# Kernel optimization log

Hardware: AMD Instinct MI355X
Metric: run time of the kernel (lower is better)

Reference implementation:

```python
import jax, jax.numpy as jnp
import numpy as np

MODEL_DIM = 512
NUM_HEADS = 8
HEAD_DIM = MODEL_DIM // NUM_HEADS  # 64
NUM_NODE = 1024
CLUSTER = 128
S = 60
EMBED = 0.5


def setup_inputs() -> dict:
    key = jax.random.key(0)
    ks = jax.random.split(key, 16)
    d = MODEL_DIM
    sc = 1.0 / np.sqrt(d)
    inp = {
        "x": jax.random.normal(ks[0], (4, 12, NUM_NODE, d), dtype=jnp.float32),
        "Wq": jax.random.normal(ks[1], (d, d), dtype=jnp.float32) * sc,
        "bq": jnp.zeros((d,), jnp.float32),
        "Wk": jax.random.normal(ks[2], (d, d), dtype=jnp.float32) * sc,
        "bk": jnp.zeros((d,), jnp.float32),
        "Wv": jax.random.normal(ks[3], (d, d), dtype=jnp.float32) * sc,
        "bv": jnp.zeros((d,), jnp.float32),
        "We": jax.random.normal(ks[4], (d, d), dtype=jnp.float32) * sc,
        "be": jnp.zeros((d,), jnp.float32),
        "Wo": jax.random.normal(ks[5], (d, d), dtype=jnp.float32) * sc,
        "bo": jnp.zeros((d,), jnp.float32),
        # adp_pos is initialized to zeros in torch; use small randn for a non-degenerate test
        "adp_pos": jax.random.normal(ks[6], (NUM_NODE, CLUSTER), dtype=jnp.float32) * 0.02,
        "U1": jax.random.normal(ks[7], (HEAD_DIM, S), dtype=jnp.float32) * np.sqrt(2.0 / (HEAD_DIM + S)),
        "U2": jax.random.normal(ks[8], (S, HEAD_DIM), dtype=jnp.float32) * np.sqrt(2.0 / (S + HEAD_DIM)),
    }
    return inp


def _split_heads(t):
    # torch.cat(torch.split(t, head_dim, -1), 0): heads stacked head-major on batch dim
    return jnp.concatenate(jnp.split(t, NUM_HEADS, axis=-1), axis=0)


def _merge_heads(t):
    return jnp.concatenate(jnp.split(t, NUM_HEADS, axis=0), axis=-1)


def _pool_nodes(t):
    # AdaptiveAvgPool2d((CLUSTER, None)) on (B,T,N,D) with N % CLUSTER == 0 -> block mean
    B, T, N, D = t.shape
    return t.reshape(B, T, CLUSTER, N // CLUSTER, D).mean(axis=3)


def reference(x, Wq, bq, Wk, bk, Wv, bv, We, be, Wo, bo, adp_pos, U1, U2):
    q = x @ Wq.T + bq                      # (B,T,N,D)
    k = _pool_nodes(x @ Wk.T + bk)          # (B,T,C,D)
    v = _pool_nodes(x @ Wv.T + bv)          # (B,T,C,D)
    ev = x @ We.T + be                      # (B,T,N,D)

    qh = _split_heads(q)                    # (B*H,T,N,d)
    kh = _split_heads(k)                    # (B*H,T,C,d)
    vh = _split_heads(v)                    # (B*H,T,C,d)
    evh = _split_heads(ev)                  # (B*H,T,N,d)

    # external attention branch: softmax over node dim (-2)
    exa = jax.nn.softmax(evh @ U1, axis=-2)  # (B*H,T,N,S)
    exa_val = (exa @ U2) * EMBED + evh       # (B*H,T,N,d)

    score = jnp.einsum("btnd,btcd->btnc", qh, kh) / np.sqrt(HEAD_DIM)
    score = score + adp_pos[None, None]      # (B*H,T,N,C)
    attn = jax.nn.softmax(score, axis=-1)

    out = attn @ vh + exa_val                # (B*H,T,N,d)
    out = _merge_heads(out)                  # (B,T,N,D)
    return out @ Wo.T + bo
```

## Files before the change

kernel.cpp:

```cpp
#include <hip/hip_runtime.h>


#define LOG2E 1.44269504088896f

typedef __attribute__((ext_vector_type(4))) float f32x4;
typedef __attribute__((ext_vector_type(8))) short bf16x8;

__device__ __forceinline__ unsigned short f2bf(float f) {
    union { float f; unsigned u; } v; v.f = f;
    unsigned r = (v.u + 0x7fffu + ((v.u >> 16) & 1u)) >> 16;
    return (unsigned short)r;
}
__device__ __forceinline__ float bf2f(unsigned short h) {
    union { unsigned u; float f; } v; v.u = ((unsigned)h) << 16;
    return v.f;
}
__device__ __forceinline__ unsigned cvt_pk_bf16(float lo, float hi) {
    unsigned r;
    asm("v_cvt_pk_bf16_f32 %0, %1, %2" : "=v"(r) : "v"(lo), "v"(hi));
    return r;
}
__device__ __forceinline__ void gll16(const void* g, void* l) {
    __builtin_amdgcn_global_load_lds((const __attribute__((address_space(1))) void*)g,
                                     (__attribute__((address_space(3))) void*)l,
                                     16, 0, 0);
}

__global__ void cvt_w(const float* __restrict__ Wq, const float* __restrict__ Wk,
                      const float* __restrict__ Wv, const float* __restrict__ We,
                      const float* __restrict__ Wo, const float* __restrict__ U1,
                      const float* __restrict__ U2,
                      const float* __restrict__ bq, const float* __restrict__ bk,
                      const float* __restrict__ bv, const float* __restrict__ be,
                      unsigned short* __restrict__ Wqe, unsigned short* __restrict__ Wkv,
                      unsigned short* __restrict__ Wob, unsigned short* __restrict__ U1T,
                      unsigned short* __restrict__ U2bT,
                      float* __restrict__ bqe, float* __restrict__ bkv)
{
    int i = blockIdx.x * 256 + threadIdx.x;
    if (i < 524288) {
        int r = i >> 9;
        float v = (r < 512) ? Wq[i] * 0.125f : We[i - 262144];
        Wqe[i] = f2bf(v);
    } else if (i < 1048576) {
        int j = i - 524288; int r = j >> 9;
        float v = (r < 512) ? Wk[j] : Wv[j - 262144];
        Wkv[j] = f2bf(v);
    } else if (i < 1310720) {
        int j = i - 1048576;
        Wob[j] = f2bf(Wo[j]);
    } else if (i < 1314816) {
        int j = i - 1310720; int s = j >> 6, k = j & 63;
        U1T[j] = (s < 60) ? f2bf(U1[k * 60 + s]) : (unsigned short)0;
    } else if (i < 1318912) {
        int j = i - 1314816; int d = j >> 6, s = j & 63;
        U2bT[j] = (s < 60) ? f2bf(U2[s * 64 + d] * 0.5f) : (unsigned short)0;
    } else if (i < 1319936) {
        int j = i - 1318912;
        bqe[j] = (j < 512) ? bq[j] * 0.125f : be[j - 512];
    } else if (i < 1320960) {
        int j = i - 1319936;
        bkv[j] = (j < 512) ? bk[j] : bv[j - 512];
    }
}

__global__ void cvt_pool(const float* __restrict__ x, unsigned short* __restrict__ xb,
                         unsigned short* __restrict__ xpb)
{
    int i = blockIdx.x * 256 + threadIdx.x;
    int d4 = i & 127;
    int btc = i >> 7;
    int bt = btc >> 7, c = btc & 127;
    long base = ((long)(bt * 1024 + c * 8)) * 128 + d4;
    const float4* src = (const float4*)x + base;
    ushort4* dst = (ushort4*)xb + base;
    float sx = 0.f, sy = 0.f, sz = 0.f, sw = 0.f;
#pragma unroll
    for (int j = 0; j < 8; j++) {
        float4 v = src[(long)j * 128];
        sx += v.x; sy += v.y; sz += v.z; sw += v.w;
        ushort4 o;
        o.x = f2bf(v.x); o.y = f2bf(v.y); o.z = f2bf(v.z); o.w = f2bf(v.w);
        dst[(long)j * 128] = o;
    }
    ushort4 p;
    p.x = f2bf(sx * 0.125f); p.y = f2bf(sy * 0.125f);
    p.z = f2bf(sz * 0.125f); p.w = f2bf(sw * 0.125f);
    ((ushort4*)xpb)[(long)btc * 128 + d4] = p;
}

__global__ __launch_bounds__(256, 4) void g1_qev(
    const unsigned short* __restrict__ A, const unsigned short* __restrict__ W,
    const float* __restrict__ bias, unsigned short* __restrict__ qh,
    unsigned short* __restrict__ evh)
{
    const int K = 512;
    __shared__ __attribute__((aligned(16))) unsigned short As[128 * 32];
    __shared__ __attribute__((aligned(16))) unsigned short Bs[128 * 32];
    const int tid = threadIdx.x;
    const int wave = tid >> 6, lane = tid & 63;
    const int quad = lane >> 4, l16 = lane & 15;
    const int m0 = blockIdx.x * 128, n0 = blockIdx.y * 128;
    const int wm = (wave & 1) * 64, wn = (wave >> 1) * 64;

    f32x4 acc[4][4];
#pragma unroll
    for (int i = 0; i < 4; i++)
#pragma unroll
        for (int j = 0; j < 4; j++) acc[i][j] = (f32x4){0.f, 0.f, 0.f, 0.f};

    const int c0 = tid, c1 = tid + 256;
    const int r0 = c0 >> 2, kc0 = (c0 & 3) * 8;
    const int r1 = c1 >> 2, kc1 = (c1 & 3) * 8;
    const unsigned short* pa0 = A + (long)(m0 + r0) * K + kc0;
    const unsigned short* pa1 = A + (long)(m0 + r1) * K + kc1;
    const unsigned short* pb0 = W + (long)(n0 + r0) * K + kc0;
    const unsigned short* pb1 = W + (long)(n0 + r1) * K + kc1;
    unsigned short* lA0 = &As[wave * 512];
    unsigned short* lA1 = &As[2048 + wave * 512];
    unsigned short* lB0 = &Bs[wave * 512];
    unsigned short* lB1 = &Bs[2048 + wave * 512];

    for (int k0 = 0; k0 < K; k0 += 32) {
        gll16(pa0 + k0, lA0);
        gll16(pa1 + k0, lA1);
        gll16(pb0 + k0, lB0);
        gll16(pb1 + k0, lB1);
        __syncthreads();
        bf16x8 af[4], bfr[4];
#pragma unroll
        for (int t = 0; t < 4; t++)
            af[t] = *(const bf16x8*)&As[(wm + t * 16 + l16) * 32 + quad * 8];
#pragma unroll
        for (int t = 0; t < 4; t++)
            bfr[t] = *(const bf16x8*)&Bs[(wn + t * 16 + l16) * 32 + quad * 8];
#pragma unroll
        for (int tm = 0; tm < 4; tm++)
#pragma unroll
            for (int tn = 0; tn < 4; tn++)
                acc[tm][tn] = __builtin_amdgcn_mfma_f32_16x16x32_bf16(
                    af[tm], bfr[tn], acc[tm][tn], 0, 0, 0);
        __syncthreads();
    }

#pragma unroll
    for (int tm = 0; tm < 4; tm++)
#pragma unroll
        for (int tn = 0; tn < 4; tn++) {
            int cc = n0 + wn + tn * 16 + l16;
            float bv = bias[cc];
            int hq = (cc >> 6) & 7, dd = cc & 63;
            int rr0 = m0 + wm + tm * 16 + quad * 4;
            int bt = rr0 >> 10, n = rr0 & 1023;
            unsigned short* dst = ((cc < 512) ? qh : evh)
                + ((long)(bt * 8 + hq) * 1024 + n) * 64 + dd;
#pragma unroll
            for (int r = 0; r < 4; r++)
                dst[(long)r * 64] = f2bf(acc[tm][tn][r] + bv);
        }
}

template <int OUTF32>
__global__ __launch_bounds__(256, 4) void gemm_bt(
    const unsigned short* __restrict__ A, const unsigned short* __restrict__ W,
    const float* __restrict__ bias, void* __restrict__ Cout,
    int M, int N, int K)
{
    __shared__ __attribute__((aligned(16))) unsigned short As[128 * 32];
    __shared__ __attribute__((aligned(16))) unsigned short Bs[128 * 32];
    const int tid = threadIdx.x;
    const int wave = tid >> 6, lane = tid & 63;
    const int quad = lane >> 4, l16 = lane & 15;
    const int m0 = blockIdx.x * 128, n0 = blockIdx.y * 128;
    const int wm = (wave & 1) * 64, wn = (wave >> 1) * 64;

    f32x4 acc[4][4];
#pragma unroll
    for (int i = 0; i < 4; i++)
#pragma unroll
        for (int j = 0; j < 4; j++) acc[i][j] = (f32x4){0.f, 0.f, 0.f, 0.f};

    const int c0 = tid, c1 = tid + 256;
    const int r0 = c0 >> 2, kc0 = (c0 & 3) * 8;
    const int r1 = c1 >> 2, kc1 = (c1 & 3) * 8;
    const unsigned short* pa0 = A + (long)(m0 + r0) * K + kc0;
    const unsigned short* pa1 = A + (long)(m0 + r1) * K + kc1;
    const unsigned short* pb0 = W + (long)(n0 + r0) * K + kc0;
    const unsigned short* pb1 = W + (long)(n0 + r1) * K + kc1;
    unsigned short* lA0 = &As[wave * 512];
    unsigned short* lA1 = &As[2048 + wave * 512];
    unsigned short* lB0 = &Bs[wave * 512];
    unsigned short* lB1 = &Bs[2048 + wave * 512];

    for (int k0 = 0; k0 < K; k0 += 32) {
        gll16(pa0 + k0, lA0);
        gll16(pa1 + k0, lA1);
        gll16(pb0 + k0, lB0);
        gll16(pb1 + k0, lB1);
        __syncthreads();
        bf16x8 af[4], bfr[4];
#pragma unroll
        for (int t = 0; t < 4; t++)
            af[t] = *(const bf16x8*)&As[(wm + t * 16 + l16) * 32 + quad * 8];
#pragma unroll
        for (int t = 0; t < 4; t++)
            bfr[t] = *(const bf16x8*)&Bs[(wn + t * 16 + l16) * 32 + quad * 8];
#pragma unroll
        for (int tm = 0; tm < 4; tm++)
#pragma unroll
            for (int tn = 0; tn < 4; tn++)
                acc[tm][tn] = __builtin_amdgcn_mfma_f32_16x16x32_bf16(
                    af[tm], bfr[tn], acc[tm][tn], 0, 0, 0);
        __syncthreads();
    }

#pragma unroll
    for (int tm = 0; tm < 4; tm++)
#pragma unroll
        for (int tn = 0; tn < 4; tn++) {
            int cc = n0 + wn + tn * 16 + l16;
            float bv = bias[cc];
#pragma unroll
            for (int r = 0; r < 4; r++) {
                int rr = m0 + wm + tm * 16 + quad * 4 + r;
                float v = acc[tm][tn][r] + bv;
                if (OUTF32) ((float*)Cout)[(long)rr * N + cc] = v;
                else        ((unsigned short*)Cout)[(long)rr * N + cc] = f2bf(v);
            }
        }
}

__global__ __launch_bounds__(256, 4) void g2_kv(
    const unsigned short* __restrict__ A, const unsigned short* __restrict__ W,
    const float* __restrict__ bias, unsigned short* __restrict__ kvK,
    unsigned short* __restrict__ vT)
{
    const int K = 512;
    __shared__ __attribute__((aligned(16))) unsigned short As[128 * 32];
    __shared__ __attribute__((aligned(16))) unsigned short Bs[128 * 32];
    const int tid = threadIdx.x;
    const int wave = tid >> 6, lane = tid & 63;
    const int quad = lane >> 4, l16 = lane & 15;
    const int m0 = blockIdx.x * 128, n0 = blockIdx.y * 128;
    const int wm = (wave & 1) * 64, wn = (wave >> 1) * 64;

    f32x4 acc[4][4];
#pragma unroll
    for (int i = 0; i < 4; i++)
#pragma unroll
        for (int j = 0; j < 4; j++) acc[i][j] = (f32x4){0.f, 0.f, 0.f, 0.f};

    const int c0 = tid, c1 = tid + 256;
    const int r0 = c0 >> 2, kc0 = (c0 & 3) * 8;
    const int r1 = c1 >> 2, kc1 = (c1 & 3) * 8;
    const unsigned short* pa0 = A + (long)(m0 + r0) * K + kc0;
    const unsigned short* pa1 = A + (long)(m0 + r1) * K + kc1;
    const unsigned short* pb0 = W + (long)(n0 + r0) * K + kc0;
    const unsigned short* pb1 = W + (long)(n0 + r1) * K + kc1;
    unsigned short* lA0 = &As[wave * 512];
    unsigned short* lA1 = &As[2048 + wave * 512];
    unsigned short* lB0 = &Bs[wave * 512];
    unsigned short* lB1 = &Bs[2048 + wave * 512];

    for (int k0 = 0; k0 < K; k0 += 32) {
        gll16(pa0 + k0, lA0);
        gll16(pa1 + k0, lA1);
        gll16(pb0 + k0, lB0);
        gll16(pb1 + k0, lB1);
        __syncthreads();
        bf16x8 af[4], bfr[4];
#pragma unroll
        for (int t = 0; t < 4; t++)
            af[t] = *(const bf16x8*)&As[(wm + t * 16 + l16) * 32 + quad * 8];
#pragma unroll
        for (int t = 0; t < 4; t++)
            bfr[t] = *(const bf16x8*)&Bs[(wn + t * 16 + l16) * 32 + quad * 8];
#pragma unroll
        for (int tm = 0; tm < 4; tm++)
#pragma unroll
            for (int tn = 0; tn < 4; tn++)
                acc[tm][tn] = __builtin_amdgcn_mfma_f32_16x16x32_bf16(
                    af[tm], bfr[tn], acc[tm][tn], 0, 0, 0);
        __syncthreads();
    }

#pragma unroll
    for (int tm = 0; tm < 4; tm++)
#pragma unroll
        for (int tn = 0; tn < 4; tn++) {
            int cc = n0 + wn + tn * 16 + l16;
            float bv = bias[cc];
            int rrb = m0 + wm + tm * 16 + quad * 4;
            if (cc < 512) {
#pragma unroll
                for (int r = 0; r < 4; r++)
                    kvK[(long)(rrb + r) * 512 + cc] = f2bf(acc[tm][tn][r] + bv);
            } else {
                int hh = (cc - 512) >> 6, dd = (cc - 512) & 63;
                int btv = rrb >> 7, cv = rrb & 127;
                ushort4 o;
                o.x = f2bf(acc[tm][tn][0] + bv);
                o.y = f2bf(acc[tm][tn][1] + bv);
                o.z = f2bf(acc[tm][tn][2] + bv);
                o.w = f2bf(acc[tm][tn][3] + bv);
                *(ushort4*)(vT + ((long)(btv * 8 + hh) * 64 + dd) * 128 + cv) = o;
            }
        }
}

__global__ __launch_bounds__(256, 2) void ez_kernel(
    const unsigned short* __restrict__ evh, const unsigned short* __restrict__ U1T,
    unsigned short* __restrict__ Z)
{
    __shared__ __attribute__((aligned(16))) unsigned short evs[128 * 72];
    __shared__ __attribute__((aligned(16))) unsigned short u1s[64 * 72];
    int tid = threadIdx.x, bx = blockIdx.x;
    int bt = bx >> 6, h = (bx >> 3) & 7, nb = bx & 7;
    int wave = tid >> 6, lane = tid & 63, quad = lane >> 4, l16 = lane & 15;
    long gb = ((long)(bt * 8 + h) * 1024 + nb * 128) * 64;

#pragma unroll
    for (int i = 0; i < 4; i++) {
        int c = tid + i * 256; int row = c >> 3, kc = (c & 7) * 8;
        *(int4*)&evs[row * 72 + kc] = *(const int4*)(evh + gb + row * 64 + kc);
    }
#pragma unroll
    for (int i = 0; i < 2; i++) {
        int c = tid + i * 256; int row = c >> 3, kc = (c & 7) * 8;
        *(int4*)&u1s[row * 72 + kc] = *(const int4*)(U1T + row * 64 + kc);
    }
    __syncthreads();

    f32x4 acc[2][4];
#pragma unroll
    for (int i = 0; i < 2; i++)
#pragma unroll
        for (int t = 0; t < 4; t++) acc[i][t] = (f32x4){0.f, 0.f, 0.f, 0.f};

#pragma unroll
    for (int kt = 0; kt < 2; kt++) {
        bf16x8 a[2], b[4];
#pragma unroll
        for (int i = 0; i < 2; i++)
            a[i] = *(const bf16x8*)&evs[((wave * 2 + i) * 16 + l16) * 72 + kt * 32 + quad * 8];
#pragma unroll
        for (int t = 0; t < 4; t++)
            b[t] = *(const bf16x8*)&u1s[(t * 16 + l16) * 72 + kt * 32 + quad * 8];
#pragma unroll
        for (int i = 0; i < 2; i++)
#pragma unroll
            for (int t = 0; t < 4; t++)
                acc[i][t] = __builtin_amdgcn_mfma_f32_16x16x32_bf16(a[i], b[t], acc[i][t], 0, 0, 0);
    }

    long zb = (long)(bt * 8 + h) * 1024 + nb * 128;
#pragma unroll
    for (int i = 0; i < 2; i++)
#pragma unroll
        for (int t = 0; t < 4; t++) {
            int s = t * 16 + l16;
            if (s < 60) {
#pragma unroll
                for (int r = 0; r < 4; r++) {
                    int rr = (wave * 2 + i) * 16 + quad * 4 + r;
                    Z[(zb + rr) * 60 + s] = f2bf(acc[i][t][r]);
                }
            }
        }
}

__global__ __launch_bounds__(1024, 4) void es_kernel(
    const unsigned short* __restrict__ Z, float* __restrict__ mS, float* __restrict__ lSinv)
{
    __shared__ float ms[16][64];
    __shared__ float ls[16][64];
    int tid = threadIdx.x;
    int s = tid & 63, g = tid >> 6;
    long zb = (long)blockIdx.x * 1024 * 60;
    float m = -1e30f, l = 0.f;
    if (s < 60) {
        for (int r = 0; r < 64; r++) {
            float z = bf2f(Z[zb + (long)(g * 64 + r) * 60 + s]);
            float nm = fmaxf(m, z);
            l = l * exp2f((m - nm) * LOG2E) + exp2f((z - nm) * LOG2E);
            m = nm;
        }
    }
    ms[g][s] = m; ls[g][s] = l;
    __syncthreads();
    if (tid < 60) {
        float M = ms[0][tid];
#pragma unroll
        for (int gg = 1; gg < 16; gg++) M = fmaxf(M, ms[gg][tid]);
        float L = 0.f;
#pragma unroll
        for (int gg = 0; gg < 16; gg++) L += ls[gg][tid] * exp2f((ms[gg][tid] - M) * LOG2E);
        mS[blockIdx.x * 60 + tid] = M;
        lSinv[blockIdx.x * 60 + tid] = 1.0f / L;
    }
}

__global__ __launch_bounds__(256, 5) void att_kernel(
    const unsigned short* __restrict__ qh, const unsigned short* __restrict__ evh,
    const unsigned short* __restrict__ kvK, const unsigned short* __restrict__ vT,
    const unsigned short* __restrict__ Z,
    const float* __restrict__ mS, const float* __restrict__ lI,
    const float* __restrict__ adp, const unsigned short* __restrict__ U2bT,
    unsigned short* __restrict__ attn_out)
{
    __shared__ __attribute__((aligned(16))) unsigned short Ps[128 * 128];

    int tid = threadIdx.x, bx = blockIdx.x;
    int bt = bx >> 6, h = (bx >> 3) & 7, nb = bx & 7;
    int wave = tid >> 6, lane = tid & 63, quad = lane >> 4, l16 = lane & 15;
    int n0 = nb * 128;
    const int g = bt * 8 + h;
    const long grow0 = (long)g * 1024 + n0;

    f32x4 sc[2][8];
#pragma unroll
    for (int i = 0; i < 2; i++)
#pragma unroll
        for (int t = 0; t < 8; t++) sc[i][t] = (f32x4){0.f, 0.f, 0.f, 0.f};

#pragma unroll
    for (int kt = 0; kt < 2; kt++) {
        bf16x8 qf[2];
#pragma unroll
        for (int i = 0; i < 2; i++)
            qf[i] = *(const bf16x8*)(qh + (grow0 + wave * 32 + i * 16 + l16) * 64
                                     + kt * 32 + quad * 8);
#pragma unroll
        for (int tn = 0; tn < 8; tn++) {
            bf16x8 kf = *(const bf16x8*)(kvK + (long)(bt * 128 + tn * 16 + l16) * 512
                                         + h * 64 + kt * 32 + quad * 8);
#pragma unroll
            for (int i = 0; i < 2; i++)
                sc[i][tn] = __builtin_amdgcn_mfma_f32_16x16x32_bf16(kf, qf[i], sc[i][tn], 0, 0, 0);
        }
    }

#pragma unroll
    for (int i = 0; i < 2; i++) {
        const int qr = wave * 32 + i * 16 + l16;
        float m = -1e30f;
#pragma unroll
        for (int tn = 0; tn < 8; tn++) {
            float4 ad = *(const float4*)(adp + (long)(n0 + qr) * 128 + tn * 16 + quad * 4);
            sc[i][tn][0] += ad.x; sc[i][tn][1] += ad.y;
            sc[i][tn][2] += ad.z; sc[i][tn][3] += ad.w;
#pragma unroll
            for (int r = 0; r < 4; r++) m = fmaxf(m, sc[i][tn][r]);
        }
        m = fmaxf(m, __shfl_xor(m, 16, 64));
        m = fmaxf(m, __shfl_xor(m, 32, 64));
        float s = 0.f;
#pragma unroll
        for (int tn = 0; tn < 8; tn++)
#pragma unroll
            for (int r = 0; r < 4; r++) {
                float p = exp2f((sc[i][tn][r] - m) * LOG2E);
                sc[i][tn][r] = p; s += p;
            }
        s += __shfl_xor(s, 16, 64);
        s += __shfl_xor(s, 32, 64);
        float rinv = 1.0f / s;
#pragma unroll
        for (int tn = 0; tn < 8; tn++) {
            uint2 w2;
            w2.x = cvt_pk_bf16(sc[i][tn][0] * rinv, sc[i][tn][1] * rinv);
            w2.y = cvt_pk_bf16(sc[i][tn][2] * rinv, sc[i][tn][3] * rinv);
            unsigned wb = (unsigned)(qr * 256 + tn * 32 + quad * 8) ^ ((unsigned)(qr & 7) << 4);
            *(uint2*)((char*)Ps + wb) = w2;
        }
    }

    f32x4 oc[2][4];
#pragma unroll
    for (int i = 0; i < 2; i++)
#pragma unroll
        for (int t = 0; t < 4; t++) oc[i][t] = (f32x4){0.f, 0.f, 0.f, 0.f};

#pragma unroll
    for (int kt = 0; kt < 4; kt++) {
        bf16x8 a[2];
#pragma unroll
        for (int i = 0; i < 2; i++) {
            int row = wave * 32 + i * 16 + l16;
            unsigned rb = (unsigned)(row * 256 + kt * 64 + quad * 16) ^ ((unsigned)(row & 7) << 4);
            a[i] = *(const bf16x8*)((char*)Ps + rb);
        }
#pragma unroll
        for (int tn = 0; tn < 4; tn++) {
            bf16x8 b = *(const bf16x8*)(vT + ((long)g * 64 + tn * 16 + l16) * 128
                                        + kt * 32 + quad * 8);
#pragma unroll
            for (int i = 0; i < 2; i++)
                oc[i][tn] = __builtin_amdgcn_mfma_f32_16x16x32_bf16(a[i], b, oc[i][tn], 0, 0, 0);
        }
    }

#pragma unroll
    for (int kt = 0; kt < 2; kt++) {
        int sb = kt * 32 + quad * 8;
        float4 ma = *(const float4*)(mS + (long)g * 60 + sb);
        float4 mb2 = *(const float4*)(mS + (long)g * 60 + sb + 4);
        float4 la = *(const float4*)(lI + (long)g * 60 + sb);
        float4 lb2 = *(const float4*)(lI + (long)g * 60 + sb + 4);
        float mv[8] = {ma.x, ma.y, ma.z, ma.w, mb2.x, mb2.y, mb2.z, mb2.w};
        float lv[8] = {la.x, la.y, la.z, la.w, lb2.x, lb2.y, lb2.z, lb2.w};
        bf16x8 ea[2];
#pragma unroll
        for (int i = 0; i < 2; i++) {
            int row = (wave * 2 + i) * 16 + l16;
            const unsigned short* zp = Z + ((long)g * 1024 + n0 + row) * 60 + sb;
            uint2 z0 = *(const uint2*)zp;
            uint2 z1 = *(const uint2*)(zp + 4);
            unsigned zz[4] = {z0.x, z0.y, z1.x, z1.y};
            unsigned short es_[8];
#pragma unroll
            for (int j = 0; j < 8; j++) {
                unsigned short zh = (unsigned short)((zz[j >> 1] >> ((j & 1) * 16)) & 0xffff);
                float e = (sb + j < 60)
                    ? exp2f((bf2f(zh) - mv[j]) * LOG2E) * lv[j] : 0.f;
                es_[j] = f2bf(e);
            }
            ea[i] = *(bf16x8*)es_;
        }
#pragma unroll
        for (int tn = 0; tn < 4; tn++) {
            bf16x8 b = *(const bf16x8*)(U2bT + (tn * 16 + l16) * 64 + sb);
#pragma unroll
            for (int i = 0; i < 2; i++)
                oc[i][tn] = __builtin_amdgcn_mfma_f32_16x16x32_bf16(ea[i], b, oc[i][tn], 0, 0, 0);
        }
    }

#pragma unroll
    for (int i = 0; i < 2; i++)
#pragma unroll
        for (int tn = 0; tn < 4; tn++)
#pragma unroll
            for (int r = 0; r < 4; r++) {
                int rr = (wave * 2 + i) * 16 + quad * 4 + r;
                int cc = tn * 16 + l16;
                float ev = bf2f(evh[(grow0 + rr) * 64 + cc]);
                attn_out[((long)bt * 1024 + n0 + rr) * 512 + h * 64 + cc]
                    = f2bf(oc[i][tn][r] + ev);
            }
}

extern "C" void kernel_launch(void* const* d_in, const int* in_sizes, int n_in,
                              void* d_out, int out_size, void* d_ws, size_t ws_size,
                              hipStream_t stream)
{
    const float* x   = (const float*)d_in[0];
    const float* Wq  = (const float*)d_in[1];
    const float* bq  = (const float*)d_in[2];
    const float* Wk  = (const float*)d_in[3];
    const float* bk  = (const float*)d_in[4];
    const float* Wv  = (const float*)d_in[5];
    const float* bv  = (const float*)d_in[6];
    const float* We  = (const float*)d_in[7];
    const float* be  = (const float*)d_in[8];
    const float* Wo  = (const float*)d_in[9];
    const float* bo  = (const float*)d_in[10];
    const float* adp = (const float*)d_in[11];
    const float* U1  = (const float*)d_in[12];
    const float* U2  = (const float*)d_in[13];

    char* ws = (char*)d_ws;
    unsigned short* xb   = (unsigned short*)(ws + 0);
    unsigned short* aout = xb;
    unsigned short* xpb  = (unsigned short*)(ws + 50331648);
    unsigned short* qh   = (unsigned short*)(ws + 56623104);
    unsigned short* evh  = (unsigned short*)(ws + 106954752);
    unsigned short* kvK  = (unsigned short*)(ws + 157286400);
    unsigned short* vT   = (unsigned short*)(ws + 163577856);
    unsigned short* Zb   = (unsigned short*)(ws + 169869312);
    unsigned short* Wqe  = (unsigned short*)(ws + 217055232);
    unsigned short* Wkv  = (unsigned short*)(ws + 218103808);
    unsigned short* Wob  = (unsigned short*)(ws + 219152384);
    unsigned short* U1T  = (unsigned short*)(ws + 219676672);
    unsigned short* U2bT = (unsigned short*)(ws + 219684864);
    float*          mSb  = (float*)(ws + 219693056);
    float*          lIb  = (float*)(ws + 219785216);
    float*          bqe  = (float*)(ws + 219877376);
    float*          bkv  = (float*)(ws + 219881472);

    cvt_w<<<5160, 256, 0, stream>>>(Wq, Wk, Wv, We, Wo, U1, U2, bq, bk, bv, be,
                                    Wqe, Wkv, Wob, U1T, U2bT, bqe, bkv);
    cvt_pool<<<3072, 256, 0, stream>>>(x, xb, xpb);

    g1_qev<<<dim3(384, 8), 256, 0, stream>>>(xb, Wqe, bqe, qh, evh);
    g2_kv<<<dim3(48, 8), 256, 0, stream>>>(xpb, Wkv, bkv, kvK, vT);

    ez_kernel<<<3072, 256, 0, stream>>>(evh, U1T, Zb);
    es_kernel<<<384, 1024, 0, stream>>>(Zb, mSb, lIb);
    att_kernel<<<3072, 256, 0, stream>>>(qh, evh, kvK, vT, Zb, mSb, lIb, adp, U2bT, aout);

    gemm_bt<1><<<dim3(384, 4), 256, 0, stream>>>(aout, Wob, bo, d_out, 49152, 512, 512);
}
```

Before: 479.3 us.

## Swizzle GEMM block order per XCD, fuse softmax stats into ez, shrink attention LDS

The GEMM kernels now use a 1D grid with XCD-aware block remapping, so consecutive blocks on the same XCD share A tiles in L2. The column-softmax statistics are computed as per-block partials inside ez_kernel and merged by a small es_reduce kernel, which replaces the separate re-read of Z in es_kernel. The attention kernel halves its P LDS buffer by staging P in two halves from registers, raises occupancy on ez_kernel, and adds s_setprio around MFMA bursts. The partials reuse the xb workspace region, which is only safe because xb is dead by the time ez_kernel runs.

```diff
diff --git a/kernel.cpp b/kernel.cpp
--- a/kernel.cpp
+++ b/kernel.cpp
@@ -100,14 +100,15 @@
     const int tid = threadIdx.x;
     const int wave = tid >> 6, lane = tid & 63;
     const int quad = lane >> 4, l16 = lane & 15;
-    const int m0 = blockIdx.x * 128, n0 = blockIdx.y * 128;
+    const int b = blockIdx.x, xcd = b & 7, j = b >> 3;
+    const int m0 = (((j >> 3) << 3) + xcd) * 128, n0 = (j & 7) * 128;
     const int wm = (wave & 1) * 64, wn = (wave >> 1) * 64;
 
     f32x4 acc[4][4];
 #pragma unroll
     for (int i = 0; i < 4; i++)
 #pragma unroll
-        for (int j = 0; j < 4; j++) acc[i][j] = (f32x4){0.f, 0.f, 0.f, 0.f};
+        for (int jj = 0; jj < 4; jj++) acc[i][jj] = (f32x4){0.f, 0.f, 0.f, 0.f};
 
     const int c0 = tid, c1 = tid + 256;
     const int r0 = c0 >> 2, kc0 = (c0 & 3) * 8;
@@ -160,25 +161,27 @@
         }
 }
 
-template <int OUTF32>
+template <int NTL2>
 __global__ __launch_bounds__(256, 4) void gemm_bt(
     const unsigned short* __restrict__ A, const unsigned short* __restrict__ W,
-    const float* __restrict__ bias, void* __restrict__ Cout,
-    int M, int N, int K)
+    const float* __restrict__ bias, float* __restrict__ Cout,
+    int N, int K)
 {
     __shared__ __attribute__((aligned(16))) unsigned short As[128 * 32];
     __shared__ __attribute__((aligned(16))) unsigned short Bs[128 * 32];
     const int tid = threadIdx.x;
     const int wave = tid >> 6, lane = tid & 63;
     const int quad = lane >> 4, l16 = lane & 15;
-    const int m0 = blockIdx.x * 128, n0 = blockIdx.y * 128;
+    const int b = blockIdx.x, xcd = b & 7, j = b >> 3;
+    const int m0 = (((j >> NTL2) << 3) + xcd) * 128;
+    const int n0 = (j & ((1 << NTL2) - 1)) * 128;
     const int wm = (wave & 1) * 64, wn = (wave >> 1) * 64;
 
     f32x4 acc[4][4];
 #pragma unroll
     for (int i = 0; i < 4; i++)
 #pragma unroll
-        for (int j = 0; j < 4; j++) acc[i][j] = (f32x4){0.f, 0.f, 0.f, 0.f};
+        for (int jj = 0; jj < 4; jj++) acc[i][jj] = (f32x4){0.f, 0.f, 0.f, 0.f};
 
     const int c0 = tid, c1 = tid + 256;
     const int r0 = c0 >> 2, kc0 = (c0 & 3) * 8;
@@ -223,9 +226,7 @@
 #pragma unroll
             for (int r = 0; r < 4; r++) {
                 int rr = m0 + wm + tm * 16 + quad * 4 + r;
-                float v = acc[tm][tn][r] + bv;
-                if (OUTF32) ((float*)Cout)[(long)rr * N + cc] = v;
-                else        ((unsigned short*)Cout)[(long)rr * N + cc] = f2bf(v);
+                Cout[(long)rr * N + cc] = acc[tm][tn][r] + bv;
             }
         }
 }
@@ -241,14 +242,15 @@
     const int tid = threadIdx.x;
     const int wave = tid >> 6, lane = tid & 63;
     const int quad = lane >> 4, l16 = lane & 15;
-    const int m0 = blockIdx.x * 128, n0 = blockIdx.y * 128;
+    const int b = blockIdx.x, xcd = b & 7, j = b >> 3;
+    const int m0 = (((j >> 3) << 3) + xcd) * 128, n0 = (j & 7) * 128;
     const int wm = (wave & 1) * 64, wn = (wave >> 1) * 64;
 
     f32x4 acc[4][4];
 #pragma unroll
     for (int i = 0; i < 4; i++)
 #pragma unroll
-        for (int j = 0; j < 4; j++) acc[i][j] = (f32x4){0.f, 0.f, 0.f, 0.f};
+        for (int jj = 0; jj < 4; jj++) acc[i][jj] = (f32x4){0.f, 0.f, 0.f, 0.f};
 
     const int c0 = tid, c1 = tid + 256;
     const int r0 = c0 >> 2, kc0 = (c0 & 3) * 8;
@@ -308,12 +310,14 @@
         }
 }
 
-__global__ __launch_bounds__(256, 2) void ez_kernel(
+__global__ __launch_bounds__(256, 4) void ez_kernel(
     const unsigned short* __restrict__ evh, const unsigned short* __restrict__ U1T,
-    unsigned short* __restrict__ Z)
+    unsigned short* __restrict__ Z, float* __restrict__ pM, float* __restrict__ pL)
 {
     __shared__ __attribute__((aligned(16))) unsigned short evs[128 * 72];
     __shared__ __attribute__((aligned(16))) unsigned short u1s[64 * 72];
+    __shared__ float ms4[4][64];
+    __shared__ float ls4[4][64];
     int tid = threadIdx.x, bx = blockIdx.x;
     int bt = bx >> 6, h = (bx >> 3) & 7, nb = bx & 7;
     int wave = tid >> 6, lane = tid & 63, quad = lane >> 4, l16 = lane & 15;
@@ -354,49 +358,85 @@
     }
 
     long zb = (long)(bt * 8 + h) * 1024 + nb * 128;
+    unsigned short zr[2][4][4];
 #pragma unroll
     for (int i = 0; i < 2; i++)
 #pragma unroll
         for (int t = 0; t < 4; t++) {
             int s = t * 16 + l16;
+#pragma unroll
+            for (int r = 0; r < 4; r++) zr[i][t][r] = f2bf(acc[i][t][r]);
             if (s < 60) {
 #pragma unroll
                 for (int r = 0; r < 4; r++) {
                     int rr = (wave * 2 + i) * 16 + quad * 4 + r;
-                    Z[(zb + rr) * 60 + s] = f2bf(acc[i][t][r]);
+                    Z[(zb + rr) * 60 + s] = zr[i][t][r];
                 }
             }
         }
-}
-
-__global__ __launch_bounds__(1024, 4) void es_kernel(
-    const unsigned short* __restrict__ Z, float* __restrict__ mS, float* __restrict__ lSinv)
-{
-    __shared__ float ms[16][64];
-    __shared__ float ls[16][64];
-    int tid = threadIdx.x;
-    int s = tid & 63, g = tid >> 6;
-    long zb = (long)blockIdx.x * 1024 * 60;
-    float m = -1e30f, l = 0.f;
+
+    float mp[4], lp[4];
+#pragma unroll
+    for (int t = 0; t < 4; t++) {
+        float m = -1e30f;
+#pragma unroll
+        for (int i = 0; i < 2; i++)
+#pragma unroll
+            for (int r = 0; r < 4; r++) m = fmaxf(m, bf2f(zr[i][t][r]));
+        float l = 0.f;
+#pragma unroll
+        for (int i = 0; i < 2; i++)
+#pragma unroll
+            for (int r = 0; r < 4; r++) l += exp2f((bf2f(zr[i][t][r]) - m) * LOG2E);
+        mp[t] = m; lp[t] = l;
+    }
+#pragma unroll
+    for (int d = 16; d <= 32; d <<= 1)
+#pragma unroll
+        for (int t = 0; t < 4; t++) {
+            float mo = __shfl_xor(mp[t], d, 64);
+            float lo = __shfl_xor(lp[t], d, 64);
+            float nm = fmaxf(mp[t], mo);
+            lp[t] = lp[t] * exp2f((mp[t] - nm) * LOG2E) + lo * exp2f((mo - nm) * LOG2E);
+            mp[t] = nm;
+        }
+    if (quad == 0) {
+#pragma unroll
+        for (int t = 0; t < 4; t++) {
+            ms4[wave][t * 16 + l16] = mp[t];
+            ls4[wave][t * 16 + l16] = lp[t];
+        }
+    }
+    __syncthreads();
+    if (tid < 64) {
+        float M = ms4[0][tid];
+#pragma unroll
+        for (int w = 1; w < 4; w++) M = fmaxf(M, ms4[w][tid]);
+        float L = 0.f;
+#pragma unroll
+        for (int w = 0; w < 4; w++) L += ls4[w][tid] * exp2f((ms4[w][tid] - M) * LOG2E);
+        pM[(long)bx * 64 + tid] = M;
+        pL[(long)bx * 64 + tid] = L;
+    }
+}
+
+__global__ void es_reduce(const float* __restrict__ pM, const float* __restrict__ pL,
+                          float* __restrict__ mS, float* __restrict__ lSinv)
+{
+    int g = blockIdx.x, s = threadIdx.x;
+    float mv[8], lv[8], M = -1e30f;
+#pragma unroll
+    for (int nb = 0; nb < 8; nb++) {
+        mv[nb] = pM[(long)(g * 8 + nb) * 64 + s];
+        lv[nb] = pL[(long)(g * 8 + nb) * 64 + s];
+        M = fmaxf(M, mv[nb]);
+    }
+    float L = 0.f;
+#pragma unroll
+    for (int nb = 0; nb < 8; nb++) L += lv[nb] * exp2f((mv[nb] - M) * LOG2E);
     if (s < 60) {
-        for (int r = 0; r < 64; r++) {
-            float z = bf2f(Z[zb + (long)(g * 64 + r) * 60 + s]);
-            float nm = fmaxf(m, z);
-            l = l * exp2f((m - nm) * LOG2E) + exp2f((z - nm) * LOG2E);
-            m = nm;
-        }
-    }
-    ms[g][s] = m; ls[g][s] = l;
-    __syncthreads();
-    if (tid < 60) {
-        float M = ms[0][tid];
-#pragma unroll
-        for (int gg = 1; gg < 16; gg++) M = fmaxf(M, ms[gg][tid]);
-        float L = 0.f;
-#pragma unroll
-        for (int gg = 0; gg < 16; gg++) L += ls[gg][tid] * exp2f((ms[gg][tid] - M) * LOG2E);
-        mS[blockIdx.x * 60 + tid] = M;
-        lSinv[blockIdx.x * 60 + tid] = 1.0f / L;
+        mS[g * 60 + s] = M;
+        lSinv[g * 60 + s] = 1.0f / L;
     }
 }
 
@@ -408,7 +448,7 @@
     const float* __restrict__ adp, const unsigned short* __restrict__ U2bT,
     unsigned short* __restrict__ attn_out)
 {
-    __shared__ __attribute__((aligned(16))) unsigned short Ps[128 * 128];
+    __shared__ __attribute__((aligned(16))) unsigned short Ps[128 * 64];
 
     int tid = threadIdx.x, bx = blockIdx.x;
     int bt = bx >> 6, h = (bx >> 3) & 7, nb = bx & 7;
@@ -440,6 +480,7 @@
         }
     }
 
+    uint2 pw[2][8];
 #pragma unroll
     for (int i = 0; i < 2; i++) {
         const int qr = wave * 32 + i * 16 + l16;
@@ -467,39 +508,12 @@
         float rinv = 1.0f / s;
 #pragma unroll
         for (int tn = 0; tn < 8; tn++) {
-            uint2 w2;
-            w2.x = cvt_pk_bf16(sc[i][tn][0] * rinv, sc[i][tn][1] * rinv);
-            w2.y = cvt_pk_bf16(sc[i][tn][2] * rinv, sc[i][tn][3] * rinv);
-            unsigned wb = (unsigned)(qr * 256 + tn * 32 + quad * 8) ^ ((unsigned)(qr & 7) << 4);
-            *(uint2*)((char*)Ps + wb) = w2;
-        }
-    }
-
-    f32x4 oc[2][4];
-#pragma unroll
-    for (int i = 0; i < 2; i++)
-#pragma unroll
-        for (int t = 0; t < 4; t++) oc[i][t] = (f32x4){0.f, 0.f, 0.f, 0.f};
-
-#pragma unroll
-    for (int kt = 0; kt < 4; kt++) {
-        bf16x8 a[2];
-#pragma unroll
-        for (int i = 0; i < 2; i++) {
-            int row = wave * 32 + i * 16 + l16;
-            unsigned rb = (unsigned)(row * 256 + kt * 64 + quad * 16) ^ ((unsigned)(row & 7) << 4);
-            a[i] = *(const bf16x8*)((char*)Ps + rb);
-        }
-#pragma unroll
-        for (int tn = 0; tn < 4; tn++) {
-            bf16x8 b = *(const bf16x8*)(vT + ((long)g * 64 + tn * 16 + l16) * 128
-                                        + kt * 32 + quad * 8);
-#pragma unroll
-            for (int i = 0; i < 2; i++)
-                oc[i][tn] = __builtin_amdgcn_mfma_f32_16x16x32_bf16(a[i], b, oc[i][tn], 0, 0, 0);
-        }
-    }
-
+            pw[i][tn].x = cvt_pk_bf16(sc[i][tn][0] * rinv, sc[i][tn][1] * rinv);
+            pw[i][tn].y = cvt_pk_bf16(sc[i][tn][2] * rinv, sc[i][tn][3] * rinv);
+        }
+    }
+
+    bf16x8 eav[2][2];
 #pragma unroll
     for (int kt = 0; kt < 2; kt++) {
         int sb = kt * 32 + quad * 8;
@@ -509,31 +523,79 @@
         float4 lb2 = *(const float4*)(lI + (long)g * 60 + sb + 4);
         float mv[8] = {ma.x, ma.y, ma.z, ma.w, mb2.x, mb2.y, mb2.z, mb2.w};
         float lv[8] = {la.x, la.y, la.z, la.w, lb2.x, lb2.y, lb2.z, lb2.w};
-        bf16x8 ea[2];
 #pragma unroll
         for (int i = 0; i < 2; i++) {
-            int row = (wave * 2 + i) * 16 + l16;
+            int row = wave * 32 + i * 16 + l16;
             const unsigned short* zp = Z + ((long)g * 1024 + n0 + row) * 60 + sb;
             uint2 z0 = *(const uint2*)zp;
             uint2 z1 = *(const uint2*)(zp + 4);
             unsigned zz[4] = {z0.x, z0.y, z1.x, z1.y};
             unsigned short es_[8];
 #pragma unroll
-            for (int j = 0; j < 8; j++) {
-                unsigned short zh = (unsigned short)((zz[j >> 1] >> ((j & 1) * 16)) & 0xffff);
-                float e = (sb + j < 60)
-                    ? exp2f((bf2f(zh) - mv[j]) * LOG2E) * lv[j] : 0.f;
-                es_[j] = f2bf(e);
-            }
-            ea[i] = *(bf16x8*)es_;
-        }
+            for (int jj = 0; jj < 8; jj++) {
+                unsigned short zh = (unsigned short)((zz[jj >> 1] >> ((jj & 1) * 16)) & 0xffff);
+                float e = (sb + jj < 60)
+                    ? exp2f((bf2f(zh) - mv[jj]) * LOG2E) * lv[jj] : 0.f;
+                es_[jj] = f2bf(e);
+            }
+            eav[kt][i] = *(bf16x8*)es_;
+        }
+    }
+
+    f32x4 oc[2][4];
+#pragma unroll
+    for (int i = 0; i < 2; i++)
+#pragma unroll
+        for (int t = 0; t < 4; t++) oc[i][t] = (f32x4){0.f, 0.f, 0.f, 0.f};
+
+#pragma unroll
+    for (int half = 0; half < 2; half++) {
+#pragma unroll
+        for (int i = 0; i < 2; i++) {
+            const int qr = wave * 32 + i * 16 + l16;
+#pragma unroll
+            for (int tnl = 0; tnl < 4; tnl++) {
+                unsigned wb = (unsigned)(qr * 128 + tnl * 32 + quad * 8)
+                            ^ ((unsigned)(qr & 7) << 4);
+                *(uint2*)((char*)Ps + wb) = pw[i][half * 4 + tnl];
+            }
+        }
+#pragma unroll
+        for (int ktl = 0; ktl < 2; ktl++) {
+            int kt = half * 2 + ktl;
+            bf16x8 a[2];
+#pragma unroll
+            for (int i = 0; i < 2; i++) {
+                int row = wave * 32 + i * 16 + l16;
+                unsigned rb = (unsigned)(row * 128 + ktl * 64 + quad * 16)
+                            ^ ((unsigned)(row & 7) << 4);
+                a[i] = *(const bf16x8*)((char*)Ps + rb);
+            }
+            __builtin_amdgcn_s_setprio(1);
+#pragma unroll
+            for (int tn = 0; tn < 4; tn++) {
+                bf16x8 b = *(const bf16x8*)(vT + ((long)g * 64 + tn * 16 + l16) * 128
+                                            + kt * 32 + quad * 8);
+#pragma unroll
+                for (int i = 0; i < 2; i++)
+                    oc[i][tn] = __builtin_amdgcn_mfma_f32_16x16x32_bf16(a[i], b, oc[i][tn], 0, 0, 0);
+            }
+            __builtin_amdgcn_s_setprio(0);
+        }
+    }
+
+#pragma unroll
+    for (int kt = 0; kt < 2; kt++) {
+        int sb = kt * 32 + quad * 8;
+        __builtin_amdgcn_s_setprio(1);
 #pragma unroll
         for (int tn = 0; tn < 4; tn++) {
             bf16x8 b = *(const bf16x8*)(U2bT + (tn * 16 + l16) * 64 + sb);
 #pragma unroll
             for (int i = 0; i < 2; i++)
-                oc[i][tn] = __builtin_amdgcn_mfma_f32_16x16x32_bf16(ea[i], b, oc[i][tn], 0, 0, 0);
-        }
+                oc[i][tn] = __builtin_amdgcn_mfma_f32_16x16x32_bf16(eav[kt][i], b, oc[i][tn], 0, 0, 0);
+        }
+        __builtin_amdgcn_s_setprio(0);
     }
 
 #pragma unroll
@@ -542,7 +604,7 @@
         for (int tn = 0; tn < 4; tn++)
 #pragma unroll
             for (int r = 0; r < 4; r++) {
-                int rr = (wave * 2 + i) * 16 + quad * 4 + r;
+                int rr = wave * 32 + i * 16 + quad * 4 + r;
                 int cc = tn * 16 + l16;
                 float ev = bf2f(evh[(grow0 + rr) * 64 + cc]);
                 attn_out[((long)bt * 1024 + n0 + rr) * 512 + h * 64 + cc]
@@ -572,6 +634,8 @@
     char* ws = (char*)d_ws;
     unsigned short* xb   = (unsigned short*)(ws + 0);
     unsigned short* aout = xb;
+    float*          pMb  = (float*)(ws + 0);
+    float*          pLb  = (float*)(ws + 786432);
     unsigned short* xpb  = (unsigned short*)(ws + 50331648);
     unsigned short* qh   = (unsigned short*)(ws + 56623104);
     unsigned short* evh  = (unsigned short*)(ws + 106954752);
@@ -592,12 +656,12 @@
                                     Wqe, Wkv, Wob, U1T, U2bT, bqe, bkv);
     cvt_pool<<<3072, 256, 0, stream>>>(x, xb, xpb);
 
-    g1_qev<<<dim3(384, 8), 256, 0, stream>>>(xb, Wqe, bqe, qh, evh);
-    g2_kv<<<dim3(48, 8), 256, 0, stream>>>(xpb, Wkv, bkv, kvK, vT);
-
-    ez_kernel<<<3072, 256, 0, stream>>>(evh, U1T, Zb);
-    es_kernel<<<384, 1024, 0, stream>>>(Zb, mSb, lIb);
+    g1_qev<<<3072, 256, 0, stream>>>(xb, Wqe, bqe, qh, evh);
+    g2_kv<<<384, 256, 0, stream>>>(xpb, Wkv, bkv, kvK, vT);
+
+    ez_kernel<<<3072, 256, 0, stream>>>(evh, U1T, Zb, pMb, pLb);
+    es_reduce<<<384, 64, 0, stream>>>(pMb, pLb, mSb, lIb);
     att_kernel<<<3072, 256, 0, stream>>>(qh, evh, kvK, vT, Zb, mSb, lIb, adp, U2bT, aout);
 
-    gemm_bt<1><<<dim3(384, 4), 256, 0, stream>>>(aout, Wob, bo, d_out, 49152, 512, 512);
-}
+    gemm_bt<2><<<1536, 256, 0, stream>>>(aout, Wob, bo, (float*)d_out, 512, 512);
+}
```

Result: slower. 489.3 us (+2.1%).
